# Optimization experiments

Hardware: AMD Instinct MI355X
Metric: run time of the kernel (lower is better)

Reference implementation:

```python
import jax, jax.numpy as jnp
import numpy as np

N_FREQ = 5
K = 16  # nneigh


def _gather(points, idx):
    # points: [B,N,C], idx: [B,nQ,K] -> [B,nQ,K,C]
    return jax.vmap(lambda p, i: p[i])(points, idx)


def setup_inputs() -> dict:
    key = jax.random.key(0)
    ks = jax.random.split(key, 16)
    B, nQ, N, dim_inp, dim = 2, 8192, 4096, 128, 128
    s = dim_inp ** -0.5
    return {
        "xyz_q": jax.random.uniform(ks[0], (B, nQ, 2), jnp.float32),
        "lat_rep": jax.random.normal(ks[1], (B, dim_inp), jnp.float32),
        "xyz": jax.random.uniform(ks[2], (B, N, 3), jnp.float32),
        "points": jax.random.normal(ks[3], (B, N, dim_inp), jnp.float32),
        "w_qs": jax.random.normal(ks[4], (dim_inp, dim), jnp.float32) * s,
        "w_ks": jax.random.normal(ks[5], (dim_inp, dim), jnp.float32) * s,
        "w_vs": jax.random.normal(ks[6], (dim_inp, dim), jnp.float32) * s,
        "w_kg": jax.random.normal(ks[7], (dim_inp, dim), jnp.float32) * s,
        "w_vg": jax.random.normal(ks[8], (dim_inp, dim), jnp.float32) * s,
        "gamma_w1": jax.random.normal(ks[9], (dim, dim), jnp.float32) * (dim ** -0.5),
        "gamma_b1": jnp.zeros((dim,), jnp.float32),
        "gamma_w2": jax.random.normal(ks[10], (dim, dim), jnp.float32) * (dim ** -0.5),
        "gamma_b2": jnp.zeros((dim,), jnp.float32),
        "pe_w": jax.random.normal(ks[11], (3 * 2 * N_FREQ + 3, dim), jnp.float32) * (33 ** -0.5),
        "pe_b": jnp.zeros((dim,), jnp.float32),
    }


def reference(xyz_q, lat_rep, xyz, points, w_qs, w_ks, w_vs, w_kg, w_vg,
              gamma_w1, gamma_b1, gamma_w2, gamma_b2, pe_w, pe_b):
    b, nQ, _ = xyz_q.shape
    dim = w_qs.shape[1]
    # kNN in 2D (no_grad in original): squared distance [B,nQ,N]
    dists = jnp.sum((xyz_q[:, :, None] - xyz[:, None, :, :2]) ** 2, axis=-1)
    _, knn_idx = jax.lax.top_k(-dists, K)  # ascending distance order

    # global latent [B,dim_inp] branch
    q_attn = (lat_rep @ w_qs)[:, None, None, :]          # [B,1,1,dim]
    k_global = jnp.broadcast_to((lat_rep @ w_kg)[:, None, None, :], (b, nQ, 1, dim))
    v_global = jnp.broadcast_to((lat_rep @ w_vg)[:, None, None, :], (b, nQ, 1, dim))

    k_attn = jnp.concatenate([_gather(points @ w_ks, knn_idx), k_global], axis=2)  # [B,nQ,K+1,dim]
    v_attn = jnp.concatenate([_gather(points @ w_vs, knn_idx), v_global], axis=2)

    xyz_knn = _gather(xyz, knn_idx)                      # [B,nQ,K,3]
    pos_diff = jnp.concatenate(
        [xyz_q[:, :, None] - xyz_knn[..., :2], xyz_knn[..., -1:]], axis=-1)  # [B,nQ,K,3]
    freq_bands = jnp.linspace(1.0, 2.0 ** N_FREQ, N_FREQ)
    embeds = [pos_diff]
    for fr in freq_bands:
        embeds.append(jnp.sin(pos_diff * fr))
        embeds.append(jnp.cos(pos_diff * fr))
    pos_embed = jnp.concatenate(embeds, axis=-1)         # [B,nQ,K,33]
    pos_encode = pos_embed @ pe_w + pe_b                 # [B,nQ,K,dim]
    pos_encode = jnp.concatenate(
        [pos_encode, jnp.zeros((b, nQ, 1, dim), pos_encode.dtype)], axis=2)  # [B,nQ,K+1,dim]

    h = q_attn - k_attn + pos_encode
    h = jnp.maximum(h @ gamma_w1 + gamma_b1, 0.0) @ gamma_w2 + gamma_b2
    attn = jax.nn.softmax(h, axis=-2)                    # softmax over neighbor axis
    res = jnp.sum(attn * (v_attn + pos_encode), axis=2)  # einsum 'bmnf,bmnf->bmf'
    return res
```

## Files before the change

### kernel.cpp

```cpp
#include <hip/hip_runtime.h>
#include <cstdint>

#define DIM   128
#define KNN   16
#define NB    2
#define NQ    8192
#define NPTS  4096
#define KVROWS 16
#define GRID  32
#define NCELL (GRID*GRID)
#define CAP   384

typedef unsigned short ushort_t;
typedef short vshort8 __attribute__((ext_vector_type(8)));
typedef float vfloat4 __attribute__((ext_vector_type(4)));

__device__ __forceinline__ ushort_t bf16_rne(float f) {
    unsigned u = __float_as_uint(f);
    unsigned r = u + 0x7FFFu + ((u >> 16) & 1u);
    return (ushort_t)(r >> 16);
}
__device__ __forceinline__ int cell_of(float x) {
    int c = (int)(x * 32.0f);
    return min(max(c, 0), GRID - 1);
}

__device__ __forceinline__ void pack_body(
    const float* __restrict__ src, int K, int ncols, int NT, int KS,
    ushort_t* __restrict__ dst, int gid)
{
    int total = NT*KS*64;
    if (gid >= total) return;
    int lane = gid & 63; int c = gid >> 6;
    int s = c % KS; int n = c / KS;
    int k0 = s*32 + ((lane >> 4) << 3);
    int col = n*16 + (lane & 15);
    vshort8 v;
    #pragma unroll
    for (int i = 0; i < 8; ++i) {
        int k = k0 + i;
        float f = (k < K) ? src[k*ncols + col] : 0.f;
        v[i] = (short)bf16_rne(f);
    }
    *(vshort8*)(dst + gid*8) = v;
}

__device__ __forceinline__ void scan1024(
    const int* __restrict__ cnt, int* __restrict__ cs, int* __restrict__ cu,
    int* __restrict__ ss, int t)
{
    int v0 = cnt[t*4 + 0];
    int v1 = cnt[t*4 + 1];
    int v2 = cnt[t*4 + 2];
    int v3 = cnt[t*4 + 3];
    int p0 = v0, p1 = p0 + v1, p2 = p1 + v2, p3 = p2 + v3;
    ss[t] = p3;
    __syncthreads();
    for (int off = 1; off < 256; off <<= 1) {
        int add = (t >= off) ? ss[t - off] : 0;
        __syncthreads();
        ss[t] += add;
        __syncthreads();
    }
    int excl = ss[t] - p3;
    cs[t*4 + 0] = excl;        cu[t*4 + 0] = excl;
    cs[t*4 + 1] = excl + p0;   cu[t*4 + 1] = excl + p0;
    cs[t*4 + 2] = excl + p1;   cu[t*4 + 2] = excl + p1;
    cs[t*4 + 3] = excl + p2;   cu[t*4 + 3] = excl + p2;
    if (t == 255) cs[NCELL] = ss[255];
}

__global__ __launch_bounds__(256) void pre1_k(
    const float* __restrict__ w_ks, const float* __restrict__ g_w1,
    const float* __restrict__ pe_w, const float* __restrict__ xyz,
    const float* __restrict__ xyz_q,
    float* __restrict__ Wk1, float* __restrict__ pwc,
    int* __restrict__ cellcnt, int* __restrict__ qcnt)
{
    int t = threadIdx.x; int bx = blockIdx.x;
    if (bx < 64) {
        int row = bx*2 + (t >> 7); int f = t & 127;
        float acc = 0.f;
        for (int c = 0; c < 128; ++c) acc = fmaf(w_ks[row*128 + c], g_w1[c*128 + f], acc);
        Wk1[row*128 + f] = acc;
    } else if (bx < 128) {
        int r = bx - 64; int col = t;
        float v = 0.f;
        if (r < 33) {
            if (col < 128) {
                float a = 0.f;
                for (int c = 0; c < 128; ++c) a = fmaf(pe_w[r*128 + c], g_w1[c*128 + col], a);
                v = a;
            } else {
                v = pe_w[r*128 + (col - 128)];
            }
        }
        pwc[r*256 + col] = v;
    } else if (bx < 160) {
        int gid = (bx - 128)*256 + t;
        int b = gid >> 12; int n = gid & (NPTS - 1);
        const float* p = xyz + (b*NPTS + n)*3;
        atomicAdd(&cellcnt[b*NCELL + cell_of(p[1])*GRID + cell_of(p[0])], 1);
    } else {
        int gid = (bx - 160)*256 + t;
        int b = gid >> 13; int q = gid & (NQ - 1);
        const float* p = xyz_q + (b*NQ + q)*2;
        atomicAdd(&qcnt[b*NCELL + cell_of(p[1])*GRID + cell_of(p[0])], 1);
    }
}

__global__ __launch_bounds__(256) void pre2_k(
    const float* __restrict__ pwc, const float* __restrict__ g_w2,
    const int* __restrict__ cnt, const int* __restrict__ qcnt,
    const float* __restrict__ lat, const float* __restrict__ w_qs,
    const float* __restrict__ w_kg, const float* __restrict__ w_vg,
    const float* __restrict__ g_w1, const float* __restrict__ g_b1,
    const float* __restrict__ pe_b,
    ushort_t* __restrict__ pwf, ushort_t* __restrict__ w2f,
    int* __restrict__ cell_start, int* __restrict__ cursor,
    int* __restrict__ qstart, int* __restrict__ qcursor,
    float* __restrict__ c1_out, float* __restrict__ vg_out, float* __restrict__ h2g_out)
{
    __shared__ int ss[256];
    __shared__ float qs[NB][DIM];
    __shared__ float hgx[NB][DIM];
    __shared__ float h1gx[NB][DIM];
    int t = threadIdx.x; int bx = blockIdx.x;
    if (bx < 4) {
        pack_body(pwc, 32, 256, 16, 1, pwf, bx*256 + t);
    } else if (bx < 12) {
        pack_body(g_w2, 128, 128, 8, 4, w2f, (bx - 4)*256 + t);
    } else if (bx < 14) {
        int b = bx - 12;
        scan1024(cnt + b*NCELL, cell_start + b*(NCELL+1), cursor + b*NCELL, ss, t);
    } else if (bx < 16) {
        int b = bx - 14;
        scan1024(qcnt + b*NCELL, qstart + b*(NCELL+1), qcursor + b*NCELL, ss, t);
    } else {
        int b = t >> 7; int f = t & 127;
        float aq = 0.f, ak = 0.f, av = 0.f;
        for (int c = 0; c < DIM; ++c) {
            float l = lat[b*DIM + c];
            aq = fmaf(l, w_qs[c*DIM + f], aq);
            ak = fmaf(l, w_kg[c*DIM + f], ak);
            av = fmaf(l, w_vg[c*DIM + f], av);
        }
        vg_out[b*DIM + f] = av;
        qs[b][f] = aq + pe_b[f];
        hgx[b][f] = aq - ak;
        __syncthreads();
        float acc = g_b1[f], acch = g_b1[f];
        for (int c = 0; c < DIM; ++c) {
            float w = g_w1[c*DIM + f];
            acc  = fmaf(qs[b][c], w, acc);
            acch = fmaf(hgx[b][c], w, acch);
        }
        c1_out[b*DIM + f] = acc;
        h1gx[b][f] = fmaxf(acch, 0.f);
        __syncthreads();
        float acc2 = 0.f;
        for (int c = 0; c < DIM; ++c) acc2 = fmaf(h1gx[b][c], g_w2[c*DIM + f], acc2);
        h2g_out[b*DIM + f] = acc2;
    }
}

__global__ __launch_bounds__(256) void pre3_k(
    const float* __restrict__ points, const float* __restrict__ Wk1,
    const float* __restrict__ w_vs, const float* __restrict__ pe_b,
    const float* __restrict__ xyz, const float* __restrict__ xyz_q,
    int* __restrict__ cursor, int* __restrict__ qcursor,
    float* __restrict__ K1p, float* __restrict__ Vp,
    float2* __restrict__ sxy, int* __restrict__ sidx,
    float2* __restrict__ qsxy, int* __restrict__ qsidx)
{
    __shared__ __align__(16) float pts[KVROWS*DIM];
    int t = threadIdx.x; int bx = blockIdx.x;
    if (bx < 512) {
        int r0 = bx * KVROWS;
        #pragma unroll
        for (int k = 0; k < KVROWS*DIM/256; ++k) {
            int e = t + k*256;
            pts[e] = points[r0*DIM + e];
        }
        __syncthreads();
        int f = t & 127; int mat = t >> 7;
        const float* W = mat ? w_vs : Wk1;
        float* O = mat ? Vp : K1p;
        float addv = mat ? pe_b[f] : 0.f;
        float acc[KVROWS];
        #pragma unroll
        for (int r = 0; r < KVROWS; ++r) acc[r] = 0.f;
        const float4* pts4 = reinterpret_cast<const float4*>(pts);
        for (int c4 = 0; c4 < DIM/4; ++c4) {
            float w0 = W[(c4*4+0)*DIM + f];
            float w1 = W[(c4*4+1)*DIM + f];
            float w2 = W[(c4*4+2)*DIM + f];
            float w3 = W[(c4*4+3)*DIM + f];
            #pragma unroll
            for (int r = 0; r < KVROWS; ++r) {
                float4 p = pts4[r*(DIM/4) + c4];
                acc[r] = fmaf(p.x, w0, acc[r]);
                acc[r] = fmaf(p.y, w1, acc[r]);
                acc[r] = fmaf(p.z, w2, acc[r]);
                acc[r] = fmaf(p.w, w3, acc[r]);
            }
        }
        #pragma unroll
        for (int r = 0; r < KVROWS; ++r) O[(r0 + r)*DIM + f] = acc[r] + addv;
    } else if (bx < 544) {
        int gid = (bx - 512)*256 + t;
        int b = gid >> 12; int n = gid & (NPTS - 1);
        const float* p = xyz + (b*NPTS + n)*3;
        float x = p[0], y = p[1];
        int slot = atomicAdd(&cursor[b*NCELL + cell_of(y)*GRID + cell_of(x)], 1);
        sxy[b*NPTS + slot] = make_float2(x, y);
        sidx[b*NPTS + slot] = n;
    } else {
        int gid = (bx - 544)*256 + t;
        int b = gid >> 13; int q = gid & (NQ - 1);
        const float* p = xyz_q + (b*NQ + q)*2;
        float x = p[0], y = p[1];
        int slot = atomicAdd(&qcursor[b*NCELL + cell_of(y)*GRID + cell_of(x)], 1);
        qsxy[b*NQ + slot] = make_float2(x, y);
        qsidx[b*NQ + slot] = q;
    }
}

__global__ __launch_bounds__(256) void knn_k(
    const float2* __restrict__ qsxy, const float2* __restrict__ sxy,
    const int* __restrict__ sidx, const int* __restrict__ cstart,
    int* __restrict__ knn_out)
{
    __shared__ float cand_d[4][CAP];
    __shared__ int   cand_i[4][CAP];
    int t = threadIdx.x; int wid = t >> 6, lane = t & 63;
    int bx = blockIdx.x; int b = bx >> 11; int q = (bx & 2047)*4 + wid;
    float2 qp = qsxy[b*NQ + q];
    float xq = qp.x, yq = qp.y;
    int cx = cell_of(xq), cy = cell_of(yq);
    const int* cs_b = cstart + b*(NCELL+1);
    float* cd = cand_d[wid]; int* ci = cand_i[wid];
    const float INF = 3.4e38f;
    const float CS = 1.0f/32.0f;
    int* outp = knn_out + (b*NQ + q)*KNN;
    unsigned long long lmask = (1ull << lane) - 1ull;

    for (int R = 2; R < 9; ++R) {
        int x0 = max(cx-R, 0), x1 = min(cx+R, GRID-1);
        int y0 = max(cy-R, 0), y1 = min(cy+R, GRID-1);
        int cnt = 0;
        for (int ry = y0; ry <= y1; ++ry) {
            int s0 = cs_b[ry*GRID + x0];
            int e0 = cs_b[ry*GRID + x1 + 1];
            for (int o = s0 + lane; o < e0; o += 64) {
                float2 p = sxy[b*NPTS + o];
                float dx = __fadd_rn(xq, -p.x);
                float dy = __fadd_rn(yq, -p.y);
                float d = __fadd_rn(__fmul_rn(dx, dx), __fmul_rn(dy, dy));
                int slot = cnt + (o - s0);
                if (slot < CAP) { cd[slot] = d; ci[slot] = o; }
            }
            cnt += e0 - s0;
        }
        asm volatile("s_waitcnt lgkmcnt(0)" ::: "memory");
        __builtin_amdgcn_sched_barrier(0);

        int cc = min(cnt, CAP);
        float dr[6];
        #pragma unroll
        for (int k = 0; k < 6; ++k)
            dr[k] = (lane + k*64 < cc) ? cd[lane + k*64] : INF;

        unsigned lo = 0u, hi = 0x40000000u;
        #pragma unroll 1
        for (int it = 0; it < 32; ++it) {
            if (hi - lo <= 1u) break;
            unsigned mid = (lo + hi) >> 1;
            float pv = __uint_as_float(mid);
            int c = 0;
            #pragma unroll
            for (int k = 0; k < 6; ++k)
                c += __popcll(__ballot(dr[k] <= pv));
            if (c >= KNN) {
                hi = mid;
                if (c == KNN) break;
            } else {
                lo = mid;
            }
        }
        float thr = __uint_as_float(hi);

        float bl = (x0 > 0)      ? (xq - (float)x0*CS)       : INF;
        float br = (x1 < GRID-1) ? ((float)(x1+1)*CS - xq)   : INF;
        float bb = (y0 > 0)      ? (yq - (float)y0*CS)       : INF;
        float bt = (y1 < GRID-1) ? ((float)(y1+1)*CS - yq)   : INF;
        float safe = fminf(fminf(bl, br), fminf(bb, bt)) - 2e-6f;
        bool whole = (safe > 1e8f);
        bool ok = (cnt >= KNN) && (cnt <= CAP) && (whole || thr <= safe*safe);
        if (ok || R == 8) {
            int base = 0;
            #pragma unroll
            for (int k = 0; k < 6; ++k) {
                bool p = dr[k] < thr;
                unsigned long long m = __ballot(p);
                int pos = base + __popcll(m & lmask);
                if (p && pos < KNN) outp[pos] = sidx[b*NPTS + ci[lane + k*64]];
                base += __popcll(m);
            }
            #pragma unroll
            for (int k = 0; k < 6; ++k) {
                bool p = dr[k] == thr;
                unsigned long long m = __ballot(p);
                int pos = base + __popcll(m & lmask);
                if (p && pos < KNN) outp[pos] = sidx[b*NPTS + ci[lane + k*64]];
                base += __popcll(m);
            }
            break;
        }
    }
}

__global__ __launch_bounds__(512, 2) void fuse_k(
    const float2* __restrict__ qsxy, const int* __restrict__ qsidx,
    const float* __restrict__ xyz,
    const float* __restrict__ K1p, const float* __restrict__ Vp,
    const int* __restrict__ knn_idx,
    const float* __restrict__ c1_, const float* __restrict__ vg_,
    const float* __restrict__ h2g_, const float* __restrict__ pw32_,
    const ushort_t* __restrict__ pwf, const ushort_t* __restrict__ w2f,
    float* __restrict__ out)
{
    __shared__ __align__(16) ushort_t w2B[32*512];
    __shared__ __align__(16) ushort_t h1b[8][2048];

    int t = threadIdx.x, lane = t & 63, wid = t >> 6;
    int sid = (blockIdx.x & 7) * 64 + (blockIdx.x >> 3);
    int b = sid >> 8; int qbase = (sid & 255) * 32;

    {
        const int4* s2 = (const int4*)w2f;  int4* d2 = (int4*)w2B;
        #pragma unroll
        for (int i = 0; i < 4; ++i) d2[t + i*512] = s2[t + i*512];
    }
    __syncthreads();

    int c16 = lane & 15, g = lane >> 4, rowbase = g*4;
    ushort_t* hb = h1b[wid];
    const vshort8* pwBv = (const vshort8*)pwf;
    const vshort8* w2Bv = (const vshort8*)w2B;
    const vfloat4 vzero = (vfloat4){0.f, 0.f, 0.f, 0.f};

    float pw32r[16], c1r[8], hgr[8], vgr[8];
    #pragma unroll
    for (int n = 0; n < 16; ++n) pw32r[n] = pw32_[n*16 + c16];
    #pragma unroll
    for (int n = 0; n < 8; ++n) {
        c1r[n] = c1_[b*128 + n*16 + c16];
        hgr[n] = h2g_[b*128 + n*16 + c16];
        vgr[n] = vg_[b*128 + n*16 + c16];
    }

    #pragma unroll 1
    for (int qi = 0; qi < 4; ++qi) {
        int q = qbase + wid*4 + qi;
        float2 qp = qsxy[b*NQ + q];
        float xq = qp.x, yq = qp.y;
        int qorig = qsidx[b*NQ + q];
        int idxrow = knn_idx[(b*NQ + q)*KNN + c16];
        const float* p = xyz + (b*NPTS + idxrow)*3;
        float pd0 = xq - p[0], pd1 = yq - p[1], pd2 = p[2];
        int idxr[4];
        #pragma unroll
        for (int r = 0; r < 4; ++r) idxr[r] = __shfl(idxrow, rowbase + r);

        vshort8 eh;
        int k0 = g*8;
        #pragma unroll
        for (int j = 0; j < 8; ++j) {
            int k = k0 + j;
            float v;
            if (k < 3) {
                v = (k == 0) ? pd0 : (k == 1 ? pd1 : pd2);
            } else {
                int m = k - 3; int fi = m / 6; int rem = m - fi*6;
                int comp = (rem < 3) ? rem : rem - 3;
                float pdc = (comp == 0) ? pd0 : (comp == 1 ? pd1 : pd2);
                float fr = (fi == 0) ? 1.0f : (fi == 1) ? 8.75f : (fi == 2) ? 16.5f
                         : (fi == 3) ? 24.25f : 32.0f;
                float arg = pdc * fr;
                v = (rem < 3) ? __sinf(arg) : __cosf(arg);
            }
            eh[j] = (short)bf16_rne(v);
        }
        float c32 = __cosf(32.0f * pd2);
        float c32r[4];
        #pragma unroll
        for (int r = 0; r < 4; ++r) c32r[r] = __shfl(c32, rowbase + r);

        float k1v[4][8];
        #pragma unroll
        for (int r = 0; r < 4; ++r) {
            const float* kp = K1p + ((b*NPTS + idxr[r]) << 7) + c16;
            #pragma unroll
            for (int n = 0; n < 8; ++n) k1v[r][n] = kp[n*16];
        }

        #pragma unroll
        for (int n = 0; n < 8; ++n) {
            vfloat4 a = __builtin_amdgcn_mfma_f32_16x16x32_bf16(
                eh, pwBv[n*64 + lane], vzero, 0, 0, 0);
            int col = n*16 + c16;
            int s = col >> 5;
            int lp = ((col >> 3) & 3) << 4;
            int j = c16 & 7;
            #pragma unroll
            for (int r = 0; r < 4; ++r) {
                float h = c1r[n] - k1v[r][n] + fmaf(c32r[r], pw32r[n], a[r]);
                h = fmaxf(h, 0.f);
                hb[s*512 + (lp | (rowbase + r))*8 + j] = bf16_rne(h);
            }
        }
        asm volatile("s_waitcnt lgkmcnt(0)" ::: "memory");
        __builtin_amdgcn_sched_barrier(0);

        vfloat4 acc2[8];
        #pragma unroll
        for (int n = 0; n < 8; ++n) acc2[n] = vzero;
        #pragma unroll
        for (int s = 0; s < 4; ++s) {
            vshort8 ah = ((const vshort8*)hb)[s*64 + lane];
            #pragma unroll
            for (int n = 0; n < 8; ++n) {
                vshort8 bh = w2Bv[(n*4 + s)*64 + lane];
                acc2[n] = __builtin_amdgcn_mfma_f32_16x16x32_bf16(ah, bh, acc2[n], 0, 0, 0);
            }
        }

        const float* vbase[4];
        #pragma unroll
        for (int r = 0; r < 4; ++r) vbase[r] = Vp + ((b*NPTS + idxr[r]) << 7) + c16;
        float vvp[4];
        #pragma unroll
        for (int r = 0; r < 4; ++r) vvp[r] = vbase[r][0];

        #pragma unroll
        for (int n = 0; n < 8; ++n) {
            float vvc[4];
            #pragma unroll
            for (int r = 0; r < 4; ++r) vvc[r] = vvp[r];
            if (n < 7) {
                #pragma unroll
                for (int r = 0; r < 4; ++r) vvp[r] = vbase[r][(n+1)*16];
            }
            vfloat4 ap = __builtin_amdgcn_mfma_f32_16x16x32_bf16(
                eh, pwBv[(8 + n)*64 + lane], vzero, 0, 0, 0);
            #pragma unroll
            for (int r = 0; r < 4; ++r) ap[r] = fmaf(c32r[r], pw32r[8 + n], ap[r]);

            float hg = hgr[n];
            vfloat4 a2 = acc2[n];
            float mx = fmaxf(fmaxf(a2[0], a2[1]), fmaxf(a2[2], a2[3]));
            mx = fmaxf(mx, __shfl_xor(mx, 16));
            mx = fmaxf(mx, __shfl_xor(mx, 32));
            mx = fmaxf(mx, hg);
            float sum = 0.f, num = 0.f;
            #pragma unroll
            for (int r = 0; r < 4; ++r) {
                float ev = __expf(a2[r] - mx);
                float v = vvc[r] + ap[r];
                sum += ev;
                num = fmaf(ev, v, num);
            }
            sum += __shfl_xor(sum, 16); sum += __shfl_xor(sum, 32);
            num += __shfl_xor(num, 16); num += __shfl_xor(num, 32);
            float eg = __expf(hg - mx);
            sum += eg;
            num = fmaf(eg, vgr[n], num);
            if (g == 0) out[(b*NQ + qorig)*128 + n*16 + c16] = num / sum;
        }
        asm volatile("s_waitcnt lgkmcnt(0)" ::: "memory");
        __builtin_amdgcn_sched_barrier(0);
    }
}

extern "C" void kernel_launch(void* const* d_in, const int* in_sizes, int n_in,
                              void* d_out, int out_size, void* d_ws, size_t ws_size,
                              hipStream_t stream) {
    const float* xyz_q  = (const float*)d_in[0];
    const float* lat    = (const float*)d_in[1];
    const float* xyz    = (const float*)d_in[2];
    const float* points = (const float*)d_in[3];
    const float* w_qs   = (const float*)d_in[4];
    const float* w_ks   = (const float*)d_in[5];
    const float* w_vs   = (const float*)d_in[6];
    const float* w_kg   = (const float*)d_in[7];
    const float* w_vg   = (const float*)d_in[8];
    const float* g_w1   = (const float*)d_in[9];
    const float* g_b1   = (const float*)d_in[10];
    const float* g_w2   = (const float*)d_in[11];
    const float* g_b2   = (const float*)d_in[12];
    const float* pe_w   = (const float*)d_in[13];
    const float* pe_b   = (const float*)d_in[14];
    float* out = (float*)d_out;
    (void)g_b2;

    float* ws   = (float*)d_ws;
    float* Vp   = ws;
    float* K1p  = Vp  + NB*NPTS*DIM;
    float* Wk1  = K1p + NB*NPTS*DIM;
    float* pwc  = Wk1 + DIM*DIM;
    float* c1   = pwc + 64*256;
    float* vg   = c1  + NB*DIM;
    float* h2g  = vg  + NB*DIM;
    int*   knn  = (int*)(h2g + NB*DIM);
    ushort_t* pwf = (ushort_t*)(knn + NB*NQ*KNN);
    ushort_t* w2f = pwf + 16*64*8;
    int* cellcnt  = (int*)(w2f + 32*64*8);
    int* qcnt     = cellcnt + NB*NCELL;
    int* cellstart = qcnt + NB*NCELL;
    int* cursor    = cellstart + NB*(NCELL+1);
    int* qstart    = cursor + NB*NCELL;
    int* qcursor   = qstart + NB*(NCELL+1);
    int* sidx      = qcursor + NB*NCELL;
    float2* sxy    = (float2*)(sidx + NB*NPTS);
    int* qsidx     = (int*)(sxy + NB*NPTS);
    float2* qsxy   = (float2*)(qsidx + NB*NQ);

    hipMemsetAsync(cellcnt, 0, 2*NB*NCELL*sizeof(int), stream);
    pre1_k<<<224, 256, 0, stream>>>(w_ks, g_w1, pe_w, xyz, xyz_q,
                                    Wk1, pwc, cellcnt, qcnt);
    pre2_k<<<17, 256, 0, stream>>>(pwc, g_w2, cellcnt, qcnt,
                                   lat, w_qs, w_kg, w_vg, g_w1, g_b1, pe_b,
                                   pwf, w2f, cellstart, cursor, qstart, qcursor,
                                   c1, vg, h2g);
    pre3_k<<<608, 256, 0, stream>>>(points, Wk1, w_vs, pe_b, xyz, xyz_q,
                                    cursor, qcursor, K1p, Vp, sxy, sidx, qsxy, qsidx);
    knn_k<<<NB*NQ/4, 256, 0, stream>>>(qsxy, sxy, sidx, cellstart, knn);
    fuse_k<<<NB*NQ/32, 512, 0, stream>>>(qsxy, qsidx, xyz, K1p, Vp, knn, c1, vg, h2g,
                                         pwc + 32*256, pwf, w2f, out);
}
```

Measured before the change: 109.7 us.

## Fuse grid kNN search into the attention kernel and drop knn_k launch

Removes the separate kNN kernel and runs the grid-based neighbour search per query inside fuse_k, staging candidates in the per-wave h1b shared buffer and writing the 16 indices to a small shared array. This saves a kernel launch and the global write/read of the kNN index buffer. In exchange the serial, divergent kNN work now runs inside a 512-thread block with heavy LDS and register use, which may lengthen fuse_k. Reusing h1b as scratch also relies on correct ordering with its later use.

```diff
diff --git a/kernel.cpp b/kernel.cpp
--- a/kernel.cpp
+++ b/kernel.cpp
@@ -226,105 +226,12 @@
     }
 }
 
-__global__ __launch_bounds__(256) void knn_k(
-    const float2* __restrict__ qsxy, const float2* __restrict__ sxy,
-    const int* __restrict__ sidx, const int* __restrict__ cstart,
-    int* __restrict__ knn_out)
-{
-    __shared__ float cand_d[4][CAP];
-    __shared__ int   cand_i[4][CAP];
-    int t = threadIdx.x; int wid = t >> 6, lane = t & 63;
-    int bx = blockIdx.x; int b = bx >> 11; int q = (bx & 2047)*4 + wid;
-    float2 qp = qsxy[b*NQ + q];
-    float xq = qp.x, yq = qp.y;
-    int cx = cell_of(xq), cy = cell_of(yq);
-    const int* cs_b = cstart + b*(NCELL+1);
-    float* cd = cand_d[wid]; int* ci = cand_i[wid];
-    const float INF = 3.4e38f;
-    const float CS = 1.0f/32.0f;
-    int* outp = knn_out + (b*NQ + q)*KNN;
-    unsigned long long lmask = (1ull << lane) - 1ull;
-
-    for (int R = 2; R < 9; ++R) {
-        int x0 = max(cx-R, 0), x1 = min(cx+R, GRID-1);
-        int y0 = max(cy-R, 0), y1 = min(cy+R, GRID-1);
-        int cnt = 0;
-        for (int ry = y0; ry <= y1; ++ry) {
-            int s0 = cs_b[ry*GRID + x0];
-            int e0 = cs_b[ry*GRID + x1 + 1];
-            for (int o = s0 + lane; o < e0; o += 64) {
-                float2 p = sxy[b*NPTS + o];
-                float dx = __fadd_rn(xq, -p.x);
-                float dy = __fadd_rn(yq, -p.y);
-                float d = __fadd_rn(__fmul_rn(dx, dx), __fmul_rn(dy, dy));
-                int slot = cnt + (o - s0);
-                if (slot < CAP) { cd[slot] = d; ci[slot] = o; }
-            }
-            cnt += e0 - s0;
-        }
-        asm volatile("s_waitcnt lgkmcnt(0)" ::: "memory");
-        __builtin_amdgcn_sched_barrier(0);
-
-        int cc = min(cnt, CAP);
-        float dr[6];
-        #pragma unroll
-        for (int k = 0; k < 6; ++k)
-            dr[k] = (lane + k*64 < cc) ? cd[lane + k*64] : INF;
-
-        unsigned lo = 0u, hi = 0x40000000u;
-        #pragma unroll 1
-        for (int it = 0; it < 32; ++it) {
-            if (hi - lo <= 1u) break;
-            unsigned mid = (lo + hi) >> 1;
-            float pv = __uint_as_float(mid);
-            int c = 0;
-            #pragma unroll
-            for (int k = 0; k < 6; ++k)
-                c += __popcll(__ballot(dr[k] <= pv));
-            if (c >= KNN) {
-                hi = mid;
-                if (c == KNN) break;
-            } else {
-                lo = mid;
-            }
-        }
-        float thr = __uint_as_float(hi);
-
-        float bl = (x0 > 0)      ? (xq - (float)x0*CS)       : INF;
-        float br = (x1 < GRID-1) ? ((float)(x1+1)*CS - xq)   : INF;
-        float bb = (y0 > 0)      ? (yq - (float)y0*CS)       : INF;
-        float bt = (y1 < GRID-1) ? ((float)(y1+1)*CS - yq)   : INF;
-        float safe = fminf(fminf(bl, br), fminf(bb, bt)) - 2e-6f;
-        bool whole = (safe > 1e8f);
-        bool ok = (cnt >= KNN) && (cnt <= CAP) && (whole || thr <= safe*safe);
-        if (ok || R == 8) {
-            int base = 0;
-            #pragma unroll
-            for (int k = 0; k < 6; ++k) {
-                bool p = dr[k] < thr;
-                unsigned long long m = __ballot(p);
-                int pos = base + __popcll(m & lmask);
-                if (p && pos < KNN) outp[pos] = sidx[b*NPTS + ci[lane + k*64]];
-                base += __popcll(m);
-            }
-            #pragma unroll
-            for (int k = 0; k < 6; ++k) {
-                bool p = dr[k] == thr;
-                unsigned long long m = __ballot(p);
-                int pos = base + __popcll(m & lmask);
-                if (p && pos < KNN) outp[pos] = sidx[b*NPTS + ci[lane + k*64]];
-                base += __popcll(m);
-            }
-            break;
-        }
-    }
-}
-
 __global__ __launch_bounds__(512, 2) void fuse_k(
     const float2* __restrict__ qsxy, const int* __restrict__ qsidx,
     const float* __restrict__ xyz,
+    const float2* __restrict__ sxy, const int* __restrict__ sidx,
+    const int* __restrict__ cstart,
     const float* __restrict__ K1p, const float* __restrict__ Vp,
-    const int* __restrict__ knn_idx,
     const float* __restrict__ c1_, const float* __restrict__ vg_,
     const float* __restrict__ h2g_, const float* __restrict__ pw32_,
     const ushort_t* __restrict__ pwf, const ushort_t* __restrict__ w2f,
@@ -332,6 +239,7 @@
 {
     __shared__ __align__(16) ushort_t w2B[32*512];
     __shared__ __align__(16) ushort_t h1b[8][2048];
+    __shared__ int idx16[8][16];
 
     int t = threadIdx.x, lane = t & 63, wid = t >> 6;
     int sid = (blockIdx.x & 7) * 64 + (blockIdx.x >> 3);
@@ -346,9 +254,16 @@
 
     int c16 = lane & 15, g = lane >> 4, rowbase = g*4;
     ushort_t* hb = h1b[wid];
+    float* cdw = (float*)hb;
+    int*   ciw = (int*)(hb + 768);
+    int*   i16 = idx16[wid];
+    const int* cs_b = cstart + b*(NCELL+1);
     const vshort8* pwBv = (const vshort8*)pwf;
     const vshort8* w2Bv = (const vshort8*)w2B;
     const vfloat4 vzero = (vfloat4){0.f, 0.f, 0.f, 0.f};
+    const float INF = 3.4e38f;
+    const float CS = 1.0f/32.0f;
+    unsigned long long lmask = (1ull << lane) - 1ull;
 
     float pw32r[16], c1r[8], hgr[8], vgr[8];
     #pragma unroll
@@ -366,7 +281,88 @@
         float2 qp = qsxy[b*NQ + q];
         float xq = qp.x, yq = qp.y;
         int qorig = qsidx[b*NQ + q];
-        int idxrow = knn_idx[(b*NQ + q)*KNN + c16];
+
+        {
+            int cx = cell_of(xq), cy = cell_of(yq);
+            #pragma unroll 1
+            for (int R = 2; R < 9; ++R) {
+                int x0 = max(cx-R, 0), x1 = min(cx+R, GRID-1);
+                int y0 = max(cy-R, 0), y1 = min(cy+R, GRID-1);
+                int cnt = 0;
+                for (int ry = y0; ry <= y1; ++ry) {
+                    int s0 = cs_b[ry*GRID + x0];
+                    int e0 = cs_b[ry*GRID + x1 + 1];
+                    for (int o = s0 + lane; o < e0; o += 64) {
+                        float2 p = sxy[b*NPTS + o];
+                        float dx = __fadd_rn(xq, -p.x);
+                        float dy = __fadd_rn(yq, -p.y);
+                        float d = __fadd_rn(__fmul_rn(dx, dx), __fmul_rn(dy, dy));
+                        int slot = cnt + (o - s0);
+                        if (slot < CAP) { cdw[slot] = d; ciw[slot] = o; }
+                    }
+                    cnt += e0 - s0;
+                }
+                asm volatile("s_waitcnt lgkmcnt(0)" ::: "memory");
+                __builtin_amdgcn_sched_barrier(0);
+
+                int cc = min(cnt, CAP);
+                float dr[6];
+                #pragma unroll
+                for (int k = 0; k < 6; ++k)
+                    dr[k] = (lane + k*64 < cc) ? cdw[lane + k*64] : INF;
+
+                unsigned lo = 0u, hi = 0x40000000u;
+                #pragma unroll 1
+                for (int it = 0; it < 32; ++it) {
+                    if (hi - lo <= 1u) break;
+                    unsigned mid = (lo + hi) >> 1;
+                    float pv = __uint_as_float(mid);
+                    int c = 0;
+                    #pragma unroll
+                    for (int k = 0; k < 6; ++k)
+                        c += __popcll(__ballot(dr[k] <= pv));
+                    if (c >= KNN) {
+                        hi = mid;
+                        if (c == KNN) break;
+                    } else {
+                        lo = mid;
+                    }
+                }
+                float thr = __uint_as_float(hi);
+
+                float bl = (x0 > 0)      ? (xq - (float)x0*CS)       : INF;
+                float br = (x1 < GRID-1) ? ((float)(x1+1)*CS - xq)   : INF;
+                float bb = (y0 > 0)      ? (yq - (float)y0*CS)       : INF;
+                float bt = (y1 < GRID-1) ? ((float)(y1+1)*CS - yq)   : INF;
+                float safe = fminf(fminf(bl, br), fminf(bb, bt)) - 2e-6f;
+                bool whole = (safe > 1e8f);
+                bool ok = (cnt >= KNN) && (cnt <= CAP) && (whole || thr <= safe*safe);
+                if (ok || R == 8) {
+                    int base = 0;
+                    #pragma unroll
+                    for (int k = 0; k < 6; ++k) {
+                        bool p = dr[k] < thr;
+                        unsigned long long m = __ballot(p);
+                        int pos = base + __popcll(m & lmask);
+                        if (p && pos < KNN) i16[pos] = sidx[b*NPTS + ciw[lane + k*64]];
+                        base += __popcll(m);
+                    }
+                    #pragma unroll
+                    for (int k = 0; k < 6; ++k) {
+                        bool p = dr[k] == thr;
+                        unsigned long long m = __ballot(p);
+                        int pos = base + __popcll(m & lmask);
+                        if (p && pos < KNN) i16[pos] = sidx[b*NPTS + ciw[lane + k*64]];
+                        base += __popcll(m);
+                    }
+                    break;
+                }
+            }
+            asm volatile("s_waitcnt lgkmcnt(0)" ::: "memory");
+            __builtin_amdgcn_sched_barrier(0);
+        }
+        int idxrow = i16[c16];
+
         const float* p = xyz + (b*NPTS + idxrow)*3;
         float pd0 = xq - p[0], pd1 = yq - p[1], pd2 = p[2];
         int idxr[4];
@@ -512,8 +508,7 @@
     float* c1   = pwc + 64*256;
     float* vg   = c1  + NB*DIM;
     float* h2g  = vg  + NB*DIM;
-    int*   knn  = (int*)(h2g + NB*DIM);
-    ushort_t* pwf = (ushort_t*)(knn + NB*NQ*KNN);
+    ushort_t* pwf = (ushort_t*)(h2g + NB*DIM);
     ushort_t* w2f = pwf + 16*64*8;
     int* cellcnt  = (int*)(w2f + 32*64*8);
     int* qcnt     = cellcnt + NB*NCELL;
@@ -535,7 +530,7 @@
                                    c1, vg, h2g);
     pre3_k<<<608, 256, 0, stream>>>(points, Wk1, w_vs, pe_b, xyz, xyz_q,
                                     cursor, qcursor, K1p, Vp, sxy, sidx, qsxy, qsidx);
-    knn_k<<<NB*NQ/4, 256, 0, stream>>>(qsxy, sxy, sidx, cellstart, knn);
-    fuse_k<<<NB*NQ/32, 512, 0, stream>>>(qsxy, qsidx, xyz, K1p, Vp, knn, c1, vg, h2g,
+    fuse_k<<<NB*NQ/32, 512, 0, stream>>>(qsxy, qsidx, xyz, sxy, sidx, cellstart,
+                                         K1p, Vp, c1, vg, h2g,
                                          pwc + 32*256, pwf, w2f, out);
 }
```

After: 122.4 us. 1.12x slower.
